# Kernel optimization log

Measured on AMD Instinct MI355X. Metric: run time of the kernel, lower is better.

## Reference

```python
import jax, jax.numpy as jnp
import numpy as np

# hyperparameters (init_kwargs)
T = 0.1
MARGIN = 0.0
NEG_IOU = 0.5
K = 2              # pos_topk
WEIGHT = 1.0
EXPONENT = 2.0
NEG_SAMPLES = 512  # neg_samples_num
START_DNS_EPOCH = 1

# static problem sizes
B, SPB, TPS = 16, 2, 4          # videos, sentences/video, targets/sentence
N, C = 64, 256                  # clips, channels
S = B * SPB                     # total sentences = 32
M = S * TPS                     # total moments = 128


def setup_inputs() -> dict:
    key = jax.random.key(0)
    k1, k2, k3, k4 = jax.random.split(key, 4)
    return {
        "video_feats": jax.random.normal(k1, (S, C, N, N), jnp.float32),
        "sents_feats": jax.random.normal(k2, (S, C), jnp.float32),
        "num_sentences": jnp.full((B,), SPB, jnp.int32),
        "num_targets": jnp.full((S,), TPS, jnp.int32),
        "iou2d": jax.random.uniform(k3, (S, N, N), jnp.float32),
        "iou2ds": jax.random.uniform(k4, (M, N, N), jnp.float32),
        "mask2d": jnp.triu(jnp.ones((N, N), bool)),  # 2D-TAN valid-proposal mask
        "epoch": 2,
    }


def _normalize(x):
    return x / jnp.maximum(jnp.linalg.norm(x, axis=-1, keepdims=True), 1e-12)


def _loss_core(video_feats, sents_feats, iou2d, iou2ds,
               num_sentences, num_targets, mask2d, epoch):
    S_, C_, N_, _ = video_feats.shape
    B_ = num_sentences.shape[0]
    M_ = iou2ds.shape[0]
    P = N_ * (N_ + 1) // 2  # number of True in upper-triangular mask2d

    # masked_select(mask2d) -> gather flat proposal positions (static size P)
    flat_idx = jnp.nonzero(mask2d.reshape(-1), size=P)[0]
    vf = video_feats.reshape(S_, C_, N_ * N_)[:, :, flat_idx]        # (S,C,P)
    vf = _normalize(vf.transpose(0, 2, 1))                            # (S,P,C)
    _ = _normalize(sents_feats)                                       # normalized but unused downstream
    iou2d_f = iou2d.reshape(S_, -1)[:, flat_idx]                      # (S,P)
    iou2ds_f = iou2ds.reshape(M_, -1)[:, flat_idx]                    # (M,P)

    scatter_m2s = jnp.repeat(jnp.arange(S_), num_targets, total_repeat_length=M_)
    scatter_s2b = jnp.repeat(jnp.arange(B_), num_sentences, total_repeat_length=S_)
    scatter_b2s = jnp.concatenate([jnp.zeros((1,), jnp.int32),
                                   jnp.cumsum(num_sentences)[:-1].astype(jnp.int32)])

    # all (ref, pos) pairs within each sentence's num_targets*K topk slots (uniform -> static)
    nK = (M_ // S_) * K
    base = (jnp.arange(S_) * nK)[:, None, None]
    i = jnp.arange(nK)
    zero = jnp.zeros((nK,), jnp.int32)
    ref_idx = (base + i[None, :, None] + zero[None, None, :]).reshape(-1)   # (E,)
    pos_idx = (base + zero[None, :, None] + i[None, None, :]).reshape(-1)   # (E,)
    scatter_e2s = jnp.repeat(jnp.arange(S_), nK * nK)                        # (E,)

    # top-K proposals per moment by IoU
    topk_idx = jax.lax.top_k(iou2ds_f, K)[1]                                 # (M,K)
    allm = vf[scatter_m2s]                                                   # (M,P,C)
    topk_vf = jnp.take_along_axis(allm, topk_idx[:, :, None], axis=1)        # (M,K,C)
    pos_vf = topk_vf.reshape(M_ * K, C_)

    intra_pos = jnp.sum(pos_vf[ref_idx] * pos_vf[pos_idx], axis=-1)          # (E,)
    bank = vf[scatter_b2s].reshape(B_ * P, C_)                               # one sentence per video
    intra_all = pos_vf @ bank.T                                              # (M*K, B*P)

    # positive mask: own-video block, refined by iou2d > neg_iou
    own = scatter_s2b[:, None] == jnp.arange(B_)[None, :]                    # (S,B)
    s2v_pos = iou2d_f > NEG_IOU                                              # (S,P)
    pos_mask = jnp.where(own[:, :, None], s2v_pos[:, None, :], False).reshape(S_, B_ * P)

    if epoch >= START_DNS_EPOCH:
        # DNS: similarity-weighted negative sampling without replacement (Gumbel top-k)
        sim = (jnp.einsum('mkc,pc->mkp', topk_vf, bank).mean(axis=1) + 1.0) * 0.5   # (M,B*P)
        fused = jax.ops.segment_sum(sim, scatter_m2s, num_segments=S_)
        fused = fused / num_targets[:, None].astype(sim.dtype)                      # per-sentence mean
        fused = jnp.where(pos_mask, 0.0, fused ** EXPONENT)                          # (S,B*P)
        logw = jnp.where(fused > 0, jnp.log(jnp.maximum(fused, 1e-30)), -jnp.inf)
        u = jax.random.uniform(jax.random.key(42), fused.shape, minval=1e-7, maxval=1.0 - 1e-7)
        gumbel = -jnp.log(-jnp.log(u))
        samp_idx = jax.lax.top_k(logw + gumbel, NEG_SAMPLES)[1]                      # (S,NEG_SAMPLES)
        neg_mask = jnp.zeros((S_, B_ * P), jnp.float32).at[
            jnp.arange(S_)[:, None], samp_idx].set(1.0)
    else:
        neg_mask = (~pos_mask).astype(jnp.float32)

    # LogCrossEntropy (InfoNCE with explicit negative mask)
    all_e = intra_all[ref_idx]            # (E, B*P)
    neg_e = neg_mask[scatter_e2s]         # (E, B*P)
    pos_logit = (intra_pos - MARGIN) / T
    neg_sum = jnp.sum(jnp.exp(all_e / T) * neg_e, axis=-1)
    loss = jnp.mean(-(pos_logit - jnp.log(jnp.exp(pos_logit) + neg_sum)))
    return loss


def reference(video_feats, sents_feats, num_sentences, num_targets,
              iou2d, iou2ds, mask2d, epoch):
    loss = _loss_core(video_feats, sents_feats, iou2d, iou2ds,
                      num_sentences, num_targets, mask2d, epoch)
    return (loss * WEIGHT, loss)
```

## Files before the change

kernel.cpp:

```cpp
#include <hip/hip_runtime.h>
#include <math.h>
#include <stdint.h>

#define S_    32
#define BV_   16
#define M_    128
#define C_    256
#define NN    4096
#define P_    2080
#define BP    33280
#define NSAMP 512
#define CHUNK 130

__device__ __forceinline__ uint32_t rotl32(uint32_t x, int n){ return (x<<n) | (x>>(32-n)); }

__device__ __forceinline__ void threefry2x32(uint32_t k0, uint32_t k1, uint32_t &x0, uint32_t &x1){
  uint32_t ks2 = k0 ^ k1 ^ 0x1BD11BDAu;
  x0 += k0; x1 += k1;
  #define TF_R(r) { x0 += x1; x1 = rotl32(x1, r); x1 ^= x0; }
  TF_R(13) TF_R(15) TF_R(26) TF_R(6)
  x0 += k1;  x1 += ks2 + 1u;
  TF_R(17) TF_R(29) TF_R(16) TF_R(24)
  x0 += ks2; x1 += k0 + 2u;
  TF_R(13) TF_R(15) TF_R(26) TF_R(6)
  x0 += k0;  x1 += k1 + 3u;
  TF_R(17) TF_R(29) TF_R(16) TF_R(24)
  x0 += k1;  x1 += ks2 + 4u;
  TF_R(13) TF_R(15) TF_R(26) TF_R(6)
  x0 += ks2; x1 += k0 + 5u;
  #undef TF_R
}

__global__ void k_lut(int* __restrict__ lut){
  int i = threadIdx.x;
  if(i < 64){
    int start = 64*i - (i*(i-1))/2;
    for(int j=i; j<64; ++j) lut[start + j - i] = i*64 + j;
  }
}

__global__ __launch_bounds__(256) void k_topk(const float* __restrict__ iou2ds,
                                              const int* __restrict__ lut,
                                              int* __restrict__ fpk){
  int m = blockIdx.x;
  const float* row = iou2ds + (size_t)m*NN;
  float v1=-1e30f, v2=-1e30f; int i1=0x7FFFFFFF, i2=0x7FFFFFFF;
  for(int p=threadIdx.x; p<P_; p+=256){
    float v = row[lut[p]];
    if(v > v1 || (v == v1 && p < i1)){ v2=v1; i2=i1; v1=v; i1=p; }
    else if(v > v2 || (v == v2 && p < i2)){ v2=v; i2=p; }
  }
  __shared__ float sv1[256], sv2[256];
  __shared__ int   si1[256], si2[256];
  sv1[threadIdx.x]=v1; sv2[threadIdx.x]=v2; si1[threadIdx.x]=i1; si2[threadIdx.x]=i2;
  for(int stp=128; stp>0; stp>>=1){
    __syncthreads();
    if((int)threadIdx.x < stp){
      float a1=sv1[threadIdx.x], a2=sv2[threadIdx.x];
      int   x1=si1[threadIdx.x], x2=si2[threadIdx.x];
      float b1=sv1[threadIdx.x+stp], b2=sv2[threadIdx.x+stp];
      int   y1=si1[threadIdx.x+stp], y2=si2[threadIdx.x+stp];
      float m1v, m2v; int m1i, m2i;
      bool aTop = (a1 > b1) || (a1 == b1 && x1 < y1);
      if(aTop){
        m1v=a1; m1i=x1;
        if((a2 > b1) || (a2 == b1 && x2 < y1)){ m2v=a2; m2i=x2; } else { m2v=b1; m2i=y1; }
      } else {
        m1v=b1; m1i=y1;
        if((b2 > a1) || (b2 == a1 && y2 < x1)){ m2v=b2; m2i=y2; } else { m2v=a1; m2i=x1; }
      }
      sv1[threadIdx.x]=m1v; sv2[threadIdx.x]=m2v; si1[threadIdx.x]=m1i; si2[threadIdx.x]=m2i;
    }
  }
  __syncthreads();
  if(threadIdx.x==0){
    fpk[m*2+0] = lut[si1[0]];
    fpk[m*2+1] = lut[si2[0]];
  }
}

__global__ __launch_bounds__(256) void k_posvf(const float* __restrict__ vfeat,
                                               const int* __restrict__ fpk,
                                               float* __restrict__ pos_vf){
  int row = blockIdx.x;
  int m = row >> 1;
  int s = m >> 2;
  int fp = fpk[row];
  int c = threadIdx.x;
  float v = vfeat[((size_t)s*C_ + c)*NN + fp];
  float ss = v*v;
  for(int o=32;o>0;o>>=1) ss += __shfl_down(ss, o, 64);
  __shared__ float wsum[4];
  int wv = threadIdx.x>>6, ln = threadIdx.x&63;
  if(ln==0) wsum[wv]=ss;
  __syncthreads();
  __shared__ float s_inv;
  if(threadIdx.x==0){
    float tot = wsum[0]+wsum[1]+wsum[2]+wsum[3];
    s_inv = 1.0f / fmaxf(sqrtf(tot), 1e-12f);
  }
  __syncthreads();
  pos_vf[(size_t)row*C_ + c] = v * s_inv;
}

__global__ __launch_bounds__(256) void k_qsumT(const float* __restrict__ pos_vf,
                                               float* __restrict__ qsumT){
  int s = blockIdx.x;
  int c = threadIdx.x;
  float a = 0.f;
  #pragma unroll
  for(int r=0;r<8;r++) a += pos_vf[(size_t)(s*8+r)*C_ + c];
  qsumT[c*32 + s] = a;
}

__global__ __launch_bounds__(256) void k_bank(const float* __restrict__ vfeat,
                                              float* __restrict__ bank){
  extern __shared__ float sm[];
  float* tile = sm;
  float* ssp  = sm + 256*65;
  float* invs = sm + 256*65 + 256;

  int i = blockIdx.x;
  int b = blockIdx.y;
  int t = threadIdx.x;
  int j = t & 63, cq = t >> 6;
  const float* basep = vfeat + (size_t)(2*b)*C_*NN + (size_t)i*64;

  float ssq = 0.f;
  for(int it=0; it<64; ++it){
    int cc = it*4 + cq;
    float v = basep[(size_t)cc*NN + j];
    tile[cc*65 + j] = v;
    ssq += v*v;
  }
  ssp[t] = ssq;
  __syncthreads();
  if(t < 64){
    float tot = ssp[t]+ssp[64+t]+ssp[128+t]+ssp[192+t];
    invs[t] = 1.0f/fmaxf(sqrtf(tot), 1e-12f);
  }
  __syncthreads();

  int start = 64*i - (i*(i-1))/2;
  for(int jj=i; jj<64; ++jj){
    size_t row = (size_t)b*P_ + start + (jj - i);
    bank[row*C_ + t] = tile[t*65 + jj] * invs[jj];
  }
}

__global__ __launch_bounds__(256) void k_fused_keys(const float* __restrict__ bank,
                                                    const float* __restrict__ qsumT,
                                                    const float* __restrict__ iou2d,
                                                    const int* __restrict__ lut,
                                                    unsigned int* __restrict__ ukey){
  __shared__ float tile[32*257];
  const int t = threadIdx.x;
  const int j = blockIdx.x*256 + t;

  float acc[32];
  #pragma unroll
  for(int s=0;s<32;s++) acc[s]=0.f;

  for(int cb=0; cb<8; ++cb){
    __syncthreads();
    #pragma unroll
    for(int it=0; it<8; ++it){
      int idx = it*256 + t;
      int jj  = idx >> 3;
      int c4  = idx & 7;
      float4 v = ((const float4*)bank)[ (size_t)(blockIdx.x*256 + jj)*64 + cb*8 + c4 ];
      tile[(c4*4+0)*257 + jj]=v.x; tile[(c4*4+1)*257 + jj]=v.y;
      tile[(c4*4+2)*257 + jj]=v.z; tile[(c4*4+3)*257 + jj]=v.w;
    }
    __syncthreads();
    const float* qb = qsumT + cb*32*32;
    #pragma unroll 2
    for(int cc=0; cc<32; ++cc){
      float v = tile[cc*257 + t];
      const float* qc = qb + cc*32;
      #pragma unroll
      for(int s=0;s<32;s++) acc[s] = fmaf(qc[s], v, acc[s]);
    }
  }

  int bv = j / P_;
  int p  = j - bv*P_;
  int fp = lut[p];
  float iou0 = iou2d[(size_t)(2*bv)*NN + fp];
  float iou1 = iou2d[(size_t)(2*bv+1)*NN + fp];

  #pragma unroll 1
  for(int s=0;s<32;s++){
    float fz = 0.0625f*acc[s] + 0.5f;
    bool pos = ((s>>1)==bv) && (((s&1)?iou1:iou0) > 0.5f);
    float val = pos ? 0.f : fz*fz;
    float key;
    if(val > 0.f){
      float logw = logf(fmaxf(val, 1e-30f));
      unsigned int f = (unsigned int)(s*BP + j);
      const unsigned int HALF = 532480u;
      bool second = f >= HALF;
      uint32_t x0 = second ? (f - HALF) : f;
      uint32_t x1 = second ? f : (f + HALF);
      threefry2x32(0u, 42u, x0, x1);
      uint32_t bits = second ? x1 : x0;
      uint32_t fb = (bits >> 9) | 0x3f800000u;
      float f01 = __uint_as_float(fb) - 1.0f;
      const float mn = 1e-7f, mx = 1.0f - 1e-7f;
      float u = fmaxf(mn, f01*(mx-mn) + mn);
      float g = -logf(-logf(u));
      key = logw + g;
    } else {
      key = -INFINITY;
    }
    unsigned int kb = __float_as_uint(key);
    kb = (kb & 0x80000000u) ? ~kb : (kb | 0x80000000u);
    ukey[(size_t)s*BP + j] = kb;
  }
}

__global__ __launch_bounds__(256) void k_select(const unsigned int* __restrict__ ukey,
                                                int* __restrict__ neglist){
  extern __shared__ unsigned int smem[];
  unsigned int* row  = smem;
  unsigned int* hist = smem + BP;
  __shared__ int s_scan[256];
  __shared__ unsigned int s_prefix;
  __shared__ int s_cntgt, s_need;

  const int s = blockIdx.x;
  const int t = threadIdx.x;
  const unsigned int* grow = ukey + (size_t)s*BP;
  int* list = neglist + s*NSAMP;

  const uint2* g2 = (const uint2*)grow;
  #pragma unroll 4
  for(int k=0; k<65; ++k){
    uint2 v = g2[t + 256*k];
    row[2*(t + 256*k)]   = v.x;
    row[2*(t + 256*k)+1] = v.y;
  }
  __syncthreads();

  unsigned int prefix = 0, pmask = 0;
  int need = NSAMP, cnt_gt = 0;

  for(int lev=0; lev<4; ++lev){
    const int shift = 24 - 8*lev;
    hist[t] = 0;
    __syncthreads();
    const int base = t*CHUNK;
    for(int k=0; k<CHUNK; ++k){
      unsigned int u = row[base + k];
      if((u & pmask) == prefix) atomicAdd(&hist[(u >> shift) & 255u], 1u);
    }
    __syncthreads();
    int v = (int)hist[t];
    s_scan[t] = v;
    __syncthreads();
    for(int off=1; off<256; off<<=1){
      int add = (t+off < 256) ? s_scan[t+off] : 0;
      __syncthreads();
      v += add;
      s_scan[t] = v;
      __syncthreads();
    }
    int Sb  = s_scan[t];
    int Sb1 = (t < 255) ? s_scan[t+1] : 0;
    if(Sb >= need && Sb1 < need){
      s_prefix = prefix | ((unsigned int)t << shift);
      s_cntgt  = cnt_gt + Sb1;
      s_need   = need - Sb1;
    }
    __syncthreads();
    prefix = s_prefix; cnt_gt = s_cntgt; need = s_need;
    pmask |= (0xFFu << shift);
    __syncthreads();
  }

  const unsigned int ustar = prefix;
  const int quota = need;

  int gtc = 0, eqc = 0;
  const int base = t*CHUNK;
  for(int k=0; k<CHUNK; ++k){
    unsigned int u = row[base + k];
    gtc += (u > ustar);
    eqc += (u == ustar);
  }
  int v = gtc; s_scan[t] = v; __syncthreads();
  for(int off=1; off<256; off<<=1){
    int add = (t >= off) ? s_scan[t-off] : 0;
    __syncthreads();
    v += add; s_scan[t] = v;
    __syncthreads();
  }
  const int gt_excl = v - gtc;
  v = eqc; s_scan[t] = v; __syncthreads();
  for(int off=1; off<256; off<<=1){
    int add = (t >= off) ? s_scan[t-off] : 0;
    __syncthreads();
    v += add; s_scan[t] = v;
    __syncthreads();
  }
  const int eq_excl = v - eqc;

  int gi = gt_excl, ei = eq_excl;
  for(int k=0; k<CHUNK; ++k){
    int jx = base + k;
    unsigned int u = row[jx];
    if(u > ustar){
      list[gi++] = jx;
    } else if(u == ustar){
      if(ei < quota) list[cnt_gt + ei] = jx;
      ei++;
    }
  }
}

__global__ __launch_bounds__(512) void k_negsum(const float* __restrict__ bank,
                                                const float* __restrict__ pos_vf,
                                                const int* __restrict__ neglist,
                                                float* __restrict__ ns){
  int s = blockIdx.x;
  int t = threadIdx.x;
  __shared__ float pv[8][C_];
  for(int idx=t; idx<8*C_; idx+=512) pv[idx>>8][idx&255] = pos_vf[(size_t)(s*8)*C_ + idx];
  __syncthreads();
  int j = neglist[s*NSAMP + t];
  const float4* bp = (const float4*)(bank + (size_t)j*C_);
  float acc[8] = {0,0,0,0,0,0,0,0};
  for(int c4=0; c4<64; ++c4){
    float4 bv = bp[c4];
    #pragma unroll
    for(int a=0;a<8;a++){
      float4 pvv = *(const float4*)&pv[a][c4*4];
      acc[a] += bv.x*pvv.x + bv.y*pvv.y + bv.z*pvv.z + bv.w*pvv.w;
    }
  }
  float e[8];
  #pragma unroll
  for(int a=0;a<8;a++){
    float v = expf(acc[a]/0.1f);
    for(int o=32;o>0;o>>=1) v += __shfl_down(v, o, 64);
    e[a] = v;
  }
  __shared__ float red[8][8];
  int wv = t>>6;
  if((t&63)==0){
    #pragma unroll
    for(int a=0;a<8;a++) red[wv][a]=e[a];
  }
  __syncthreads();
  if(t < 8){
    float tot = 0.f;
    for(int w=0; w<8; w++) tot += red[w][t];
    ns[s*8 + t] = tot;
  }
}

__global__ __launch_bounds__(64) void k_loss(const float* __restrict__ pos_vf,
                                             const float* __restrict__ ns,
                                             float* __restrict__ partial){
  int s = blockIdx.x;
  int t = threadIdx.x;
  __shared__ float pv[8][260];
  for(int idx=t; idx<8*C_; idx+=64){
    pv[idx>>8][idx&255] = pos_vf[(size_t)(s*8)*C_ + idx];
  }
  __syncthreads();
  int a = t>>3, b = t&7;
  float dot = 0.f;
  for(int c=0;c<C_;c++) dot += pv[a][c]*pv[b][c];
  float pl = dot/0.1f;
  float term = logf(expf(pl) + ns[s*8+a]) - pl;
  for(int o=32;o>0;o>>=1) term += __shfl_down(term, o, 64);
  if(t==0) partial[s]=term;
}

__global__ void k_final(const float* __restrict__ partial, float* __restrict__ out){
  int t = threadIdx.x;
  float v = (t < 32) ? partial[t] : 0.f;
  for(int o=32;o>0;o>>=1) v += __shfl_down(v, o, 64);
  if(t==0){
    float loss = v / 2048.0f;
    out[0] = loss * 1.0f;
    out[1] = loss;
  }
}

extern "C" void kernel_launch(void* const* d_in, const int* in_sizes, int n_in,
                              void* d_out, int out_size, void* d_ws, size_t ws_size,
                              hipStream_t stream) {
  const float* video_feats = (const float*)d_in[0];
  const float* iou2d  = (const float*)d_in[4];
  const float* iou2ds = (const float*)d_in[5];

  const size_t o_lut   = 0;
  const size_t o_fpk   = 8448;
  const size_t o_pvf   = 9472;
  const size_t o_qsT   = 271616;
  const size_t o_bank  = 304384;
  const size_t o_ukey  = 34383104;
  const size_t o_list  = 38642944;
  const size_t o_ns    = 38708480;
  const size_t o_part  = 38709504;
  const size_t NEED    = 38709632;
  if (ws_size < NEED) return;

  char* w = (char*)d_ws;
  int*          lut     = (int*)(w + o_lut);
  int*          fpk     = (int*)(w + o_fpk);
  float*        pos_vf  = (float*)(w + o_pvf);
  float*        qsumT   = (float*)(w + o_qsT);
  float*        bank    = (float*)(w + o_bank);
  unsigned int* ukey    = (unsigned int*)(w + o_ukey);
  int*          neglist = (int*)(w + o_list);
  float*        ns      = (float*)(w + o_ns);
  float*        part    = (float*)(w + o_part);
  float*        out     = (float*)d_out;

  static bool attr_set = false;
  if(!attr_set){
    (void)hipFuncSetAttribute((const void*)k_select,
                              hipFuncAttributeMaxDynamicSharedMemorySize,
                              (BP + 256) * 4);
    (void)hipFuncSetAttribute((const void*)k_bank,
                              hipFuncAttributeMaxDynamicSharedMemorySize,
                              (256*65 + 256 + 64) * 4);
    attr_set = true;
  }

  k_lut<<<1, 64, 0, stream>>>(lut);
  k_topk<<<128, 256, 0, stream>>>(iou2ds, lut, fpk);
  k_posvf<<<256, 256, 0, stream>>>(video_feats, fpk, pos_vf);
  k_qsumT<<<32, 256, 0, stream>>>(pos_vf, qsumT);
  k_bank<<<dim3(64,16), 256, (256*65 + 256 + 64) * 4, stream>>>(video_feats, bank);
  k_fused_keys<<<130, 256, 0, stream>>>(bank, qsumT, iou2d, lut, ukey);
  k_select<<<32, 256, (BP + 256) * 4, stream>>>(ukey, neglist);
  k_negsum<<<32, 512, 0, stream>>>(bank, pos_vf, neglist, ns);
  k_loss<<<32, 64, 0, stream>>>(pos_vf, ns, part);
  k_final<<<1, 64, 0, stream>>>(part, out);
}
```

Baseline: 191.3 us.

## Fuse small kernels, drop LUT, and rework radix-select histogram and scans

Removes the LUT kernel by computing triangular indices arithmetically, and merges posvf with qsumT and negsum with loss, which cuts the launch count from 10 to 7. The radix select now reads keys straight from global memory during the histogram passes, using per-lane replicated histograms to reduce atomic contention. Its block-wide shared-memory scans are replaced with wave shuffle scans. Keys are loaded into shared memory only for the final gather pass. The radix passes now re-read global memory, and the 66-way histogram adds extra reduction work.

New measurement: 239.1 us. +25.0%, slower.

```diff
diff --git a/kernel.cpp b/kernel.cpp
--- a/kernel.cpp
+++ b/kernel.cpp
@@ -31,24 +31,24 @@
   #undef TF_R
 }
 
-__global__ void k_lut(int* __restrict__ lut){
-  int i = threadIdx.x;
-  if(i < 64){
-    int start = 64*i - (i*(i-1))/2;
-    for(int j=i; j<64; ++j) lut[start + j - i] = i*64 + j;
-  }
+__device__ __forceinline__ void p_to_ij(int p, int &i, int &j){
+  i = (int)((129.0f - sqrtf((float)(16641 - 8*p))) * 0.5f);
+  while(64*(i+1) - ((i+1)*i)/2 <= p) ++i;
+  while(64*i - (i*(i-1))/2 > p) --i;
+  j = i + (p - (64*i - (i*(i-1))/2));
 }
 
 __global__ __launch_bounds__(256) void k_topk(const float* __restrict__ iou2ds,
-                                              const int* __restrict__ lut,
                                               int* __restrict__ fpk){
   int m = blockIdx.x;
   const float* row = iou2ds + (size_t)m*NN;
   float v1=-1e30f, v2=-1e30f; int i1=0x7FFFFFFF, i2=0x7FFFFFFF;
-  for(int p=threadIdx.x; p<P_; p+=256){
-    float v = row[lut[p]];
-    if(v > v1 || (v == v1 && p < i1)){ v2=v1; i2=i1; v1=v; i1=p; }
-    else if(v > v2 || (v == v2 && p < i2)){ v2=v; i2=p; }
+  for(int f=threadIdx.x; f<NN; f+=256){
+    int ti = f>>6, tj = f&63;
+    if(tj < ti) continue;
+    float v = row[f];
+    if(v > v1 || (v == v1 && f < i1)){ v2=v1; i2=i1; v1=v; i1=f; }
+    else if(v > v2 || (v == v2 && f < i2)){ v2=v; i2=f; }
   }
   __shared__ float sv1[256], sv2[256];
   __shared__ int   si1[256], si2[256];
@@ -74,51 +74,46 @@
   }
   __syncthreads();
   if(threadIdx.x==0){
-    fpk[m*2+0] = lut[si1[0]];
-    fpk[m*2+1] = lut[si2[0]];
-  }
-}
-
-__global__ __launch_bounds__(256) void k_posvf(const float* __restrict__ vfeat,
-                                               const int* __restrict__ fpk,
-                                               float* __restrict__ pos_vf){
-  int row = blockIdx.x;
-  int m = row >> 1;
-  int s = m >> 2;
-  int fp = fpk[row];
-  int c = threadIdx.x;
-  float v = vfeat[((size_t)s*C_ + c)*NN + fp];
-  float ss = v*v;
-  for(int o=32;o>0;o>>=1) ss += __shfl_down(ss, o, 64);
-  __shared__ float wsum[4];
-  int wv = threadIdx.x>>6, ln = threadIdx.x&63;
-  if(ln==0) wsum[wv]=ss;
-  __syncthreads();
-  __shared__ float s_inv;
-  if(threadIdx.x==0){
-    float tot = wsum[0]+wsum[1]+wsum[2]+wsum[3];
-    s_inv = 1.0f / fmaxf(sqrtf(tot), 1e-12f);
-  }
-  __syncthreads();
-  pos_vf[(size_t)row*C_ + c] = v * s_inv;
-}
-
-__global__ __launch_bounds__(256) void k_qsumT(const float* __restrict__ pos_vf,
-                                               float* __restrict__ qsumT){
+    fpk[m*2+0] = si1[0];
+    fpk[m*2+1] = si2[0];
+  }
+}
+
+__global__ __launch_bounds__(256) void k_pos(const float* __restrict__ vfeat,
+                                             const int* __restrict__ fpk,
+                                             float* __restrict__ pos_vf,
+                                             float* __restrict__ qsumT){
   int s = blockIdx.x;
   int c = threadIdx.x;
-  float a = 0.f;
-  #pragma unroll
-  for(int r=0;r<8;r++) a += pos_vf[(size_t)(s*8+r)*C_ + c];
-  qsumT[c*32 + s] = a;
+  __shared__ float wsum[4];
+  __shared__ float s_inv;
+  float qs = 0.f;
+  for(int r=0; r<8; ++r){
+    int row = s*8 + r;
+    int fp = fpk[row];
+    float v = vfeat[((size_t)s*C_ + c)*NN + fp];
+    float ss = v*v;
+    for(int o=32;o>0;o>>=1) ss += __shfl_down(ss, o, 64);
+    if((c&63)==0) wsum[c>>6]=ss;
+    __syncthreads();
+    if(c==0){
+      float tot = wsum[0]+wsum[1]+wsum[2]+wsum[3];
+      s_inv = 1.0f / fmaxf(sqrtf(tot), 1e-12f);
+    }
+    __syncthreads();
+    float pv = v * s_inv;
+    pos_vf[(size_t)row*C_ + c] = pv;
+    qs += pv;
+  }
+  qsumT[c*32 + s] = qs;
 }
 
 __global__ __launch_bounds__(256) void k_bank(const float* __restrict__ vfeat,
                                               float* __restrict__ bank){
-  extern __shared__ float sm[];
-  float* tile = sm;
-  float* ssp  = sm + 256*65;
-  float* invs = sm + 256*65 + 256;
+  extern __shared__ char dyn_sm[];
+  float* tile = (float*)dyn_sm;
+  float* ssp  = (float*)dyn_sm + 256*65;
+  float* invs = (float*)dyn_sm + 256*65 + 256;
 
   int i = blockIdx.x;
   int b = blockIdx.y;
@@ -151,11 +146,17 @@
 __global__ __launch_bounds__(256) void k_fused_keys(const float* __restrict__ bank,
                                                     const float* __restrict__ qsumT,
                                                     const float* __restrict__ iou2d,
-                                                    const int* __restrict__ lut,
                                                     unsigned int* __restrict__ ukey){
   __shared__ float tile[32*257];
   const int t = threadIdx.x;
   const int j = blockIdx.x*256 + t;
+
+  int bv = j / P_;
+  int p  = j - bv*P_;
+  int pi, pj; p_to_ij(p, pi, pj);
+  int fp = pi*64 + pj;
+  float iou0 = iou2d[(size_t)(2*bv)*NN + fp];
+  float iou1 = iou2d[(size_t)(2*bv+1)*NN + fp];
 
   float acc[32];
   #pragma unroll
@@ -182,12 +183,6 @@
       for(int s=0;s<32;s++) acc[s] = fmaf(qc[s], v, acc[s]);
     }
   }
-
-  int bv = j / P_;
-  int p  = j - bv*P_;
-  int fp = lut[p];
-  float iou0 = iou2d[(size_t)(2*bv)*NN + fp];
-  float iou1 = iou2d[(size_t)(2*bv+1)*NN + fp];
 
   #pragma unroll 1
   for(int s=0;s<32;s++){
@@ -221,52 +216,52 @@
 
 __global__ __launch_bounds__(256) void k_select(const unsigned int* __restrict__ ukey,
                                                 int* __restrict__ neglist){
-  extern __shared__ unsigned int smem[];
-  unsigned int* row  = smem;
-  unsigned int* hist = smem + BP;
-  __shared__ int s_scan[256];
+  extern __shared__ char dyn_sm[];
+  unsigned int* hist = (unsigned int*)dyn_sm;
+  unsigned int* row  = (unsigned int*)dyn_sm;
+  __shared__ int s_wave[8];
   __shared__ unsigned int s_prefix;
   __shared__ int s_cntgt, s_need;
 
   const int s = blockIdx.x;
   const int t = threadIdx.x;
+  const int lane = t & 63, wv = t >> 6;
   const unsigned int* grow = ukey + (size_t)s*BP;
   int* list = neglist + s*NSAMP;
 
-  const uint2* g2 = (const uint2*)grow;
-  #pragma unroll 4
-  for(int k=0; k<65; ++k){
-    uint2 v = g2[t + 256*k];
-    row[2*(t + 256*k)]   = v.x;
-    row[2*(t + 256*k)+1] = v.y;
-  }
-  __syncthreads();
-
   unsigned int prefix = 0, pmask = 0;
   int need = NSAMP, cnt_gt = 0;
 
   for(int lev=0; lev<4; ++lev){
     const int shift = 24 - 8*lev;
-    hist[t] = 0;
-    __syncthreads();
-    const int base = t*CHUNK;
+    for(int k=t; k<256*66; k+=256) hist[k] = 0;
+    __syncthreads();
+    #pragma unroll 2
     for(int k=0; k<CHUNK; ++k){
-      unsigned int u = row[base + k];
-      if((u & pmask) == prefix) atomicAdd(&hist[(u >> shift) & 255u], 1u);
-    }
-    __syncthreads();
-    int v = (int)hist[t];
-    s_scan[t] = v;
-    __syncthreads();
-    for(int off=1; off<256; off<<=1){
-      int add = (t+off < 256) ? s_scan[t+off] : 0;
-      __syncthreads();
-      v += add;
-      s_scan[t] = v;
-      __syncthreads();
-    }
-    int Sb  = s_scan[t];
-    int Sb1 = (t < 255) ? s_scan[t+1] : 0;
+      unsigned int u = grow[k*256 + t];
+      if((u & pmask) == prefix)
+        atomicAdd(&hist[((u >> shift) & 255u)*66 + lane], 1u);
+    }
+    __syncthreads();
+    unsigned int h = 0;
+    {
+      const unsigned int* hr = hist + t*66;
+      #pragma unroll
+      for(int c=0;c<64;c++) h += hr[c];
+    }
+    int v = (int)h;
+    #pragma unroll
+    for(int off=1; off<64; off<<=1){
+      int src = lane + off;
+      int o = __shfl(v, (src<64)?src:lane, 64);
+      v += (src<64)? o : 0;
+    }
+    if(lane==0) s_wave[wv] = v;
+    __syncthreads();
+    int tail = 0;
+    for(int w2=wv+1; w2<4; ++w2) tail += s_wave[w2];
+    int Sb  = v + tail;
+    int Sb1 = Sb - (int)h;
     if(Sb >= need && Sb1 < need){
       s_prefix = prefix | ((unsigned int)t << shift);
       s_cntgt  = cnt_gt + Sb1;
@@ -280,6 +275,10 @@
 
   const unsigned int ustar = prefix;
   const int quota = need;
+
+  #pragma unroll 4
+  for(int k=0; k<CHUNK; ++k) row[k*256 + t] = grow[k*256 + t];
+  __syncthreads();
 
   int gtc = 0, eqc = 0;
   const int base = t*CHUNK;
@@ -288,24 +287,22 @@
     gtc += (u > ustar);
     eqc += (u == ustar);
   }
-  int v = gtc; s_scan[t] = v; __syncthreads();
-  for(int off=1; off<256; off<<=1){
-    int add = (t >= off) ? s_scan[t-off] : 0;
-    __syncthreads();
-    v += add; s_scan[t] = v;
-    __syncthreads();
-  }
-  const int gt_excl = v - gtc;
-  v = eqc; s_scan[t] = v; __syncthreads();
-  for(int off=1; off<256; off<<=1){
-    int add = (t >= off) ? s_scan[t-off] : 0;
-    __syncthreads();
-    v += add; s_scan[t] = v;
-    __syncthreads();
-  }
-  const int eq_excl = v - eqc;
-
-  int gi = gt_excl, ei = eq_excl;
+  int vg = gtc, ve = eqc;
+  #pragma unroll
+  for(int off=1; off<64; off<<=1){
+    int src = lane - off;
+    int og = __shfl(vg, (src>=0)?src:lane, 64);
+    int oe = __shfl(ve, (src>=0)?src:lane, 64);
+    vg += (src>=0)? og : 0;
+    ve += (src>=0)? oe : 0;
+  }
+  if(lane==63){ s_wave[wv] = vg; s_wave[4+wv] = ve; }
+  __syncthreads();
+  int gbase = 0, ebase = 0;
+  for(int w2=0; w2<wv; ++w2){ gbase += s_wave[w2]; ebase += s_wave[4+w2]; }
+  int gi = gbase + vg - gtc;
+  int ei = ebase + ve - eqc;
+
   for(int k=0; k<CHUNK; ++k){
     int jx = base + k;
     unsigned int u = row[jx];
@@ -318,13 +315,15 @@
   }
 }
 
-__global__ __launch_bounds__(512) void k_negsum(const float* __restrict__ bank,
-                                                const float* __restrict__ pos_vf,
-                                                const int* __restrict__ neglist,
-                                                float* __restrict__ ns){
+__global__ __launch_bounds__(512) void k_negloss(const float* __restrict__ bank,
+                                                 const float* __restrict__ pos_vf,
+                                                 const int* __restrict__ neglist,
+                                                 float* __restrict__ partial){
   int s = blockIdx.x;
   int t = threadIdx.x;
-  __shared__ float pv[8][C_];
+  __shared__ float pv[8][260];
+  __shared__ float red[8][8];
+  __shared__ float ns_s[8];
   for(int idx=t; idx<8*C_; idx+=512) pv[idx>>8][idx&255] = pos_vf[(size_t)(s*8)*C_ + idx];
   __syncthreads();
   int j = neglist[s*NSAMP + t];
@@ -345,7 +344,6 @@
     for(int o=32;o>0;o>>=1) v += __shfl_down(v, o, 64);
     e[a] = v;
   }
-  __shared__ float red[8][8];
   int wv = t>>6;
   if((t&63)==0){
     #pragma unroll
@@ -355,27 +353,18 @@
   if(t < 8){
     float tot = 0.f;
     for(int w=0; w<8; w++) tot += red[w][t];
-    ns[s*8 + t] = tot;
-  }
-}
-
-__global__ __launch_bounds__(64) void k_loss(const float* __restrict__ pos_vf,
-                                             const float* __restrict__ ns,
-                                             float* __restrict__ partial){
-  int s = blockIdx.x;
-  int t = threadIdx.x;
-  __shared__ float pv[8][260];
-  for(int idx=t; idx<8*C_; idx+=64){
-    pv[idx>>8][idx&255] = pos_vf[(size_t)(s*8)*C_ + idx];
-  }
-  __syncthreads();
-  int a = t>>3, b = t&7;
-  float dot = 0.f;
-  for(int c=0;c<C_;c++) dot += pv[a][c]*pv[b][c];
-  float pl = dot/0.1f;
-  float term = logf(expf(pl) + ns[s*8+a]) - pl;
-  for(int o=32;o>0;o>>=1) term += __shfl_down(term, o, 64);
-  if(t==0) partial[s]=term;
+    ns_s[t] = tot;
+  }
+  __syncthreads();
+  if(t < 64){
+    int a = t>>3, b = t&7;
+    float dot = 0.f;
+    for(int c=0;c<C_;c++) dot += pv[a][c]*pv[b][c];
+    float pl = dot/0.1f;
+    float term = logf(expf(pl) + ns_s[a]) - pl;
+    for(int o=32;o>0;o>>=1) term += __shfl_down(term, o, 64);
+    if(t==0) partial[s]=term;
+  }
 }
 
 __global__ void k_final(const float* __restrict__ partial, float* __restrict__ out){
@@ -396,27 +385,23 @@
   const float* iou2d  = (const float*)d_in[4];
   const float* iou2ds = (const float*)d_in[5];
 
-  const size_t o_lut   = 0;
-  const size_t o_fpk   = 8448;
-  const size_t o_pvf   = 9472;
-  const size_t o_qsT   = 271616;
-  const size_t o_bank  = 304384;
-  const size_t o_ukey  = 34383104;
-  const size_t o_list  = 38642944;
-  const size_t o_ns    = 38708480;
-  const size_t o_part  = 38709504;
-  const size_t NEED    = 38709632;
+  const size_t o_fpk   = 0;
+  const size_t o_pvf   = 1024;
+  const size_t o_qsT   = 263168;
+  const size_t o_bank  = 295936;
+  const size_t o_ukey  = 34374656;
+  const size_t o_list  = 38634496;
+  const size_t o_part  = 38700032;
+  const size_t NEED    = 38700160;
   if (ws_size < NEED) return;
 
   char* w = (char*)d_ws;
-  int*          lut     = (int*)(w + o_lut);
   int*          fpk     = (int*)(w + o_fpk);
   float*        pos_vf  = (float*)(w + o_pvf);
   float*        qsumT   = (float*)(w + o_qsT);
   float*        bank    = (float*)(w + o_bank);
   unsigned int* ukey    = (unsigned int*)(w + o_ukey);
   int*          neglist = (int*)(w + o_list);
-  float*        ns      = (float*)(w + o_ns);
   float*        part    = (float*)(w + o_part);
   float*        out     = (float*)d_out;
 
@@ -424,21 +409,18 @@
   if(!attr_set){
     (void)hipFuncSetAttribute((const void*)k_select,
                               hipFuncAttributeMaxDynamicSharedMemorySize,
-                              (BP + 256) * 4);
+                              BP * 4);
     (void)hipFuncSetAttribute((const void*)k_bank,
                               hipFuncAttributeMaxDynamicSharedMemorySize,
                               (256*65 + 256 + 64) * 4);
     attr_set = true;
   }
 
-  k_lut<<<1, 64, 0, stream>>>(lut);
-  k_topk<<<128, 256, 0, stream>>>(iou2ds, lut, fpk);
-  k_posvf<<<256, 256, 0, stream>>>(video_feats, fpk, pos_vf);
-  k_qsumT<<<32, 256, 0, stream>>>(pos_vf, qsumT);
+  k_topk<<<128, 256, 0, stream>>>(iou2ds, fpk);
+  k_pos<<<32, 256, 0, stream>>>(video_feats, fpk, pos_vf, qsumT);
   k_bank<<<dim3(64,16), 256, (256*65 + 256 + 64) * 4, stream>>>(video_feats, bank);
-  k_fused_keys<<<130, 256, 0, stream>>>(bank, qsumT, iou2d, lut, ukey);
-  k_select<<<32, 256, (BP + 256) * 4, stream>>>(ukey, neglist);
-  k_negsum<<<32, 512, 0, stream>>>(bank, pos_vf, neglist, ns);
-  k_loss<<<32, 64, 0, stream>>>(pos_vf, ns, part);
+  k_fused_keys<<<130, 256, 0, stream>>>(bank, qsumT, iou2d, ukey);
+  k_select<<<32, 256, BP * 4, stream>>>(ukey, neglist);
+  k_negloss<<<32, 512, 0, stream>>>(bank, pos_vf, neglist, part);
   k_final<<<1, 64, 0, stream>>>(part, out);
 }
```
